# Performance work log

Measured on AMD Instinct MI355X. Metric: run time of the kernel, lower is better.

The kernel has to match this reference:

```python
import jax, jax.numpy as jnp
import numpy as np

B, N = 4, 20                        # batch, qubits
L = int(np.ceil(np.log2(N)))        # 5 layers, one 4x4 generator each


def setup_inputs():
    key = jax.random.key(0)
    k1, k2, k3, k4 = jax.random.split(key, 4)
    psi_re = jax.random.normal(k1, (B, 2 ** N), dtype=jnp.float32)
    psi_im = jax.random.normal(k2, (B, 2 ** N), dtype=jnp.float32)
    nrm = jnp.sqrt(jnp.sum(psi_re ** 2 + psi_im ** 2, axis=1, keepdims=True))
    psi_re, psi_im = psi_re / nrm, psi_im / nrm   # normalized quantum state
    H_re = jax.random.normal(k3, (L, 4, 4), dtype=jnp.float32)
    H_im = jax.random.normal(k4, (L, 4, 4), dtype=jnp.float32)
    return {"psi_re": psi_re, "psi_im": psi_im, "H_re": H_re, "H_im": H_im}


def _make_unitary(A):
    # torch.matrix_exp(A - A^H): expm of an anti-Hermitian generator via eigh
    G = A - A.conj().T
    w, V = jnp.linalg.eigh(-1j * G)            # G = i * Hermitian
    return (V * jnp.exp(1j * w)) @ V.conj().T  # expm(G), unitary


def _apply_gate(T, U4, axes):
    # contract 4x4 gate (reshaped [2,2,2,2]) onto two qubit axes of tensor T
    T = jnp.tensordot(U4, T, axes=((2, 3), axes))
    return jnp.moveaxis(T, (0, 1), axes)


def _gate_pairs(nq):
    pairs = [(2 * i, 2 * i + 1) for i in range(nq // 2)]
    if nq > 2:
        pairs += [(2 * i + 1, (2 * i + 2) % nq) for i in range(nq // 2)]
    return pairs


def _forward(psi_re, psi_im, H_re, H_im):
    psi = (psi_re + 1j * psi_im).astype(jnp.complex64).reshape((B,) + (2,) * N)
    H = (H_re + 1j * H_im).astype(jnp.complex64)
    state, is_dm, nq = psi, False, N
    for layer in range(L):
        U = _make_unitary(H[layer]).reshape(2, 2, 2, 2)
        Uc = U.conj()
        # _2local_conv: brick pattern of the same 2-qubit gate
        for (a, b) in _gate_pairs(nq):
            state = _apply_gate(state, U, (1 + a, 1 + b))
            if is_dm:  # density matrix: also apply U* on bra axes
                state = _apply_gate(state, Uc, (1 + nq + a, 1 + nq + b))
        # _2local_pool: measuring qubits 0..nq//2-1 with index shifting removes
        # the even-indexed qubits -> partial trace over them
        if nq >= 2:
            traced = [2 * i for i in range(nq // 2)]
            kept = [q for q in range(nq) if q not in traced]
            t, k = len(traced), len(kept)
            if is_dm:
                perm = (0,) + tuple(1 + q for q in kept) + tuple(1 + q for q in traced) \
                     + tuple(1 + nq + q for q in kept) + tuple(1 + nq + q for q in traced)
                r = jnp.transpose(state, perm).reshape(B, 2 ** k, 2 ** t, 2 ** k, 2 ** t)
                state = jnp.einsum('bitjt->bij', r).reshape((B,) + (2,) * k + (2,) * k)
            else:
                perm = (0,) + tuple(1 + q for q in traced) + tuple(1 + q for q in kept)
                p = jnp.transpose(state, perm).reshape(B, 2 ** t, 2 ** k)
                state = jnp.einsum('bti,btj->bij', p, p.conj()).reshape((B,) + (2,) * k + (2,) * k)
                is_dm = True
            nq = k
    # final state.measure(0): reduced 1-qubit density matrix, take P(outcome 0)
    r = state.reshape(B, 2, 2 ** (nq - 1), 2, 2 ** (nq - 1))
    rho0 = jnp.einsum('birjr->bij', r)
    return rho0[:, 0, 0].real


def reference(psi_re, psi_im, H_re, H_im):
    return _forward(psi_re, psi_im, H_re, H_im)
```

## Files before the change

kernel.cpp:

```cpp
#include <hip/hip_runtime.h>
#include <math.h>


__device__ __forceinline__ float2 cmul(float2 a, float2 b) {
  return make_float2(a.x * b.x - a.y * b.y, a.x * b.y + a.y * b.x);
}
__device__ __forceinline__ float2 cmadd(float2 acc, float2 a, float2 b) {
  acc.x = fmaf(a.x, b.x, fmaf(-a.y, b.y, acc.x));
  acc.y = fmaf(a.x, b.y, fmaf(a.y, b.x, acc.y));
  return acc;
}
__device__ __forceinline__ float2 cmaddc(float2 acc, float2 a, float2 b) {
  acc.x = fmaf(a.x, b.x, fmaf(a.y, b.y, acc.x));
  acc.y = fmaf(a.y, b.x, fmaf(-a.x, b.y, acc.y));
  return acc;
}
__device__ __forceinline__ int pad(int e) { return e + (e >> 4); }
__device__ __forceinline__ int ins(int x, int p) {
  return ((x >> p) << (p + 1)) | (x & ((1 << p) - 1));
}

__device__ __forceinline__ void gate4(float2& v0, float2& v1, float2& v2, float2& v3,
                                      const float2 (&U)[16]) {
  float2 n0 = cmul(U[0], v0);  n0 = cmadd(n0, U[1], v1);  n0 = cmadd(n0, U[2], v2);  n0 = cmadd(n0, U[3], v3);
  float2 n1 = cmul(U[4], v0);  n1 = cmadd(n1, U[5], v1);  n1 = cmadd(n1, U[6], v2);  n1 = cmadd(n1, U[7], v3);
  float2 n2 = cmul(U[8], v0);  n2 = cmadd(n2, U[9], v1);  n2 = cmadd(n2, U[10], v2); n2 = cmadd(n2, U[11], v3);
  float2 n3 = cmul(U[12], v0); n3 = cmadd(n3, U[13], v1); n3 = cmadd(n3, U[14], v2); n3 = cmadd(n3, U[15], v3);
  v0 = n0; v1 = n1; v2 = n2; v3 = n3;
}

template <int NG>
__device__ __forceinline__ void gate16n(float2 (&v)[16], const float2 (&U)[16]) {
#pragma unroll
  for (int g = 0; g < 4; g++)
    gate4(v[g * 4 + 0], v[g * 4 + 1], v[g * 4 + 2], v[g * 4 + 3], U);
#pragma unroll
  for (int lo = 0; lo < 4; lo++)
    gate4(v[lo], v[lo + 4], v[lo + 8], v[lo + 12], U);
  if (NG == 3) {
#pragma unroll
    for (int b3 = 0; b3 < 2; b3++)
#pragma unroll
      for (int b0 = 0; b0 < 2; b0++) {
        int j = b3 * 8 + b0;
        gate4(v[j], v[j + 2], v[j + 4], v[j + 6], U);
      }
  }
}

__device__ __forceinline__ void apply_gate_tile13(float2* t, const float2 (&U)[16],
                                                  int pa, int pb, int tid) {
  int p0 = pa < pb ? pa : pb;
  int p1 = pa < pb ? pb : pa;
  int m0 = (1 << p0) - 1, m1 = (1 << p1) - 1;
  int ia = 1 << pa, ib = 1 << pb;
#pragma unroll
  for (int g = tid; g < 2048; g += 512) {
    int idx = ((g & ~m0) << 1) | (g & m0);
    idx = ((idx & ~m1) << 1) | (idx & m1);
    int e0 = pad(idx), e1 = pad(idx | ib), e2 = pad(idx | ia), e3 = pad(idx | ia | ib);
    float2 v0 = t[e0], v1 = t[e1], v2 = t[e2], v3 = t[e3];
    gate4(v0, v1, v2, v3, U);
    t[e0] = v0; t[e1] = v1; t[e2] = v2; t[e3] = v3;
  }
}

template <int NG>
__device__ __forceinline__ void phase4_f(float2* t, const float2 (&U)[16],
                                         int q0, int q1, int q2, int q3,
                                         int o0, int o1, int o2, int o3, int tid) {
  int idx = ins(ins(ins(ins(tid, q0), q1), q2), q3);
  float2 v[16];
#pragma unroll
  for (int j = 0; j < 16; j++) {
    int off = ((j & 1) ? o0 : 0) + ((j & 2) ? o1 : 0) + ((j & 4) ? o2 : 0) + ((j & 8) ? o3 : 0);
    v[j] = t[pad(idx + off)];
  }
  gate16n<NG>(v, U);
#pragma unroll
  for (int j = 0; j < 16; j++) {
    int off = ((j & 1) ? o0 : 0) + ((j & 2) ? o1 : 0) + ((j & 4) ? o2 : 0) + ((j & 8) ? o3 : 0);
    t[pad(idx + off)] = v[j];
  }
}

template <int NG>
__device__ __forceinline__ void phase4_pool(float2* w, const float2 (&U)[16],
                                            int a_lo, int a_hi, int c_lo, int c_hi,
                                            int o0, int o1, int o2, int o3, int tid) {
  int uu = tid & 7, ss = (tid >> 3) & 7, t_lo = tid >> 6;
  int u = ins(ins(uu, a_lo), a_hi);
  int s = ins(ins(ss, c_lo), c_hi);
  int base = t_lo * 1120 + s * 35 + u;
  float2 v[16];
#pragma unroll
  for (int j = 0; j < 16; j++) {
    int off = ((j & 1) ? o0 : 0) + ((j & 2) ? o1 : 0) + ((j & 4) ? o2 : 0) + ((j & 8) ? o3 : 0);
    v[j] = w[base + off];
  }
  gate16n<NG>(v, U);
#pragma unroll
  for (int j = 0; j < 16; j++) {
    int off = ((j & 1) ? o0 : 0) + ((j & 2) ? o1 : 0) + ((j & 4) ? o2 : 0) + ((j & 8) ? o3 : 0);
    w[base + off] = v[j];
  }
}

__device__ __forceinline__ void pool_p3(float2* w, const float2 (&U)[16], int tid) {
#pragma unroll
  for (int it = 0; it < 2; it++) {
    int h = tid + it * 512;
    int uu = h & 7, ss = (h >> 3) & 15, t_lo = h >> 7;
    int base = t_lo * 1120 + (ss << 1) * 35 + (uu << 2);
    float2 v[8];
    v[0] = w[base];      v[1] = w[base + 1];
    v[4] = w[base + 2];  v[5] = w[base + 3];
    v[2] = w[base + 35]; v[3] = w[base + 36];
    v[6] = w[base + 37]; v[7] = w[base + 38];
    gate4(v[0], v[1], v[2], v[3], U);
    gate4(v[4], v[5], v[6], v[7], U);
    gate4(v[0], v[2], v[4], v[6], U);
    gate4(v[1], v[3], v[5], v[7], U);
    w[base] = v[0];      w[base + 1] = v[1];
    w[base + 2] = v[4];  w[base + 3] = v[5];
    w[base + 35] = v[2]; w[base + 36] = v[3];
    w[base + 37] = v[6]; w[base + 38] = v[7];
  }
}

__device__ __forceinline__ float2 expm16(const float* __restrict__ Hre,
                                         const float* __restrict__ Him,
                                         int l, int l16) {
  int r = l16 >> 2, c = l16 & 3;
  double tr = (double)Hre[l * 16 + r * 4 + c] - (double)Hre[l * 16 + c * 4 + r];
  double ti = (double)Him[l * 16 + r * 4 + c] + (double)Him[l * 16 + c * 4 + r];
  double a = sqrt(tr * tr + ti * ti);
  a += __shfl_xor(a, 1, 16);
  a += __shfl_xor(a, 2, 16);
  double nrm = fmax(a, __shfl_xor(a, 4, 16));
  nrm = fmax(nrm, __shfl_xor(nrm, 8, 16));
  int s = 0;
  while (nrm > 0.25 && s < 60) { nrm *= 0.5; s++; }
  double sc = ldexp(1.0, -s);
  tr *= sc; ti *= sc;
  double id = (r == c) ? 1.0 : 0.0;
  double er = id, ei = 0.0, pr = id, pi = 0.0;
  for (int k = 1; k <= 16; k++) {
    double qr = 0.0, qi = 0.0;
#pragma unroll
    for (int m = 0; m < 4; m++) {
      double pmr = __shfl(pr, r * 4 + m, 16);
      double pmi = __shfl(pi, r * 4 + m, 16);
      double tmr = __shfl(tr, m * 4 + c, 16);
      double tmi = __shfl(ti, m * 4 + c, 16);
      qr = fma(pmr, tmr, fma(-pmi, tmi, qr));
      qi = fma(pmr, tmi, fma(pmi, tmr, qi));
    }
    double inv = 1.0 / (double)k;
    pr = qr * inv; pi = qi * inv;
    er += pr; ei += pi;
  }
  for (int it = 0; it < s; it++) {
    double qr = 0.0, qi = 0.0;
#pragma unroll
    for (int m = 0; m < 4; m++) {
      double amr = __shfl(er, r * 4 + m, 16);
      double ami = __shfl(ei, r * 4 + m, 16);
      double bmr = __shfl(er, m * 4 + c, 16);
      double bmi = __shfl(ei, m * 4 + c, 16);
      qr = fma(amr, bmr, fma(-ami, bmi, qr));
      qi = fma(amr, bmi, fma(ami, bmr, qi));
    }
    er = qr; ei = qi;
  }
  return make_float2((float)er, (float)ei);
}

__global__ __launch_bounds__(512, 4) void l0_pass1(const float* __restrict__ pre,
                                                   const float* __restrict__ pim,
                                                   const float* __restrict__ Hre,
                                                   const float* __restrict__ Him,
                                                   float2* __restrict__ Umat,
                                                   float2* __restrict__ state) {
  extern __shared__ float2 tile[];
  __shared__ float2 Ush[16];
  int tid = threadIdx.x;
  int bid = blockIdx.x;
  int b = bid >> 7, hi = bid & 127;
  size_t base = ((size_t)b << 20) | ((size_t)hi << 13);
  for (int e4 = tid; e4 < 2048; e4 += 512) {
    int e = e4 << 2;
    float4 re = *(const float4*)&pre[base + e];
    float4 im = *(const float4*)&pim[base + e];
    int d = pad(e);
    tile[d] = make_float2(re.x, im.x);
    tile[d + 1] = make_float2(re.y, im.y);
    tile[d + 2] = make_float2(re.z, im.z);
    tile[d + 3] = make_float2(re.w, im.w);
  }
  {
    int wv = tid >> 6, g16 = (tid & 63) >> 4, l16 = tid & 15;
    int layer = (wv == 0) ? g16 : ((wv == 1 && g16 == 0) ? 4 : -1);
    if (layer == 0 || (bid == 0 && layer > 0)) {
      float2 ue = expm16(Hre, Him, layer, l16);
      if (layer == 0) Ush[l16] = ue;
      if (bid == 0) Umat[layer * 16 + l16] = ue;
    }
  }
  __syncthreads();
  float2 U[16];
#pragma unroll
  for (int k = 0; k < 16; k++) U[k] = Ush[k];
  phase4_f<3>(tile, U, 0, 1, 2, 3, 1, 2, 4, 8, tid);            __syncthreads();
  phase4_f<3>(tile, U, 4, 5, 6, 7, 16, 32, 64, 128, tid);       __syncthreads();
  phase4_f<3>(tile, U, 8, 9, 10, 11, 256, 512, 1024, 2048, tid);__syncthreads();
  phase4_f<2>(tile, U, 3, 4, 7, 8, 8, 16, 128, 256, tid);       __syncthreads();
  int hifix = ((hi & 1) << 16) | (((hi >> 1) & 1) << 6) | (((hi >> 2) & 1) << 17)
            | (((hi >> 3) & 1) << 5) | (((hi >> 4) & 1) << 18) | (((hi >> 5) & 1) << 7)
            | (((hi >> 6) & 1) << 19);
  size_t dbase = ((size_t)b << 20) | (unsigned)hifix;
  for (int e4 = tid; e4 < 2048; e4 += 512) {
    int le = e4;
    int d = ((le & 1) << 2) | (((le >> 1) & 1) << 3) | (((le >> 2) & 1) << 8)
          | (((le >> 3) & 1) << 12) | (((le >> 4) & 1) << 10) | (((le >> 5) & 1) << 13)
          | (((le >> 6) & 1) << 9) | (((le >> 7) & 1) << 14) | (((le >> 8) & 1) << 11)
          | (((le >> 9) & 1) << 15) | (((le >> 10) & 1) << 4);
    int src = pad(e4 << 2);
    float2 x0 = tile[src], x1 = tile[src + 1], x2 = tile[src + 2], x3 = tile[src + 3];
    float4* dst = (float4*)&state[dbase + d];
    dst[0] = make_float4(x0.x, x0.y, x1.x, x1.y);
    dst[1] = make_float4(x2.x, x2.y, x3.x, x3.y);
  }
}

__global__ __launch_bounds__(512, 4) void l0_pass2(const float2* __restrict__ Umat,
                                                   float2* __restrict__ state) {
  extern __shared__ float2 tile[];
  int tid = threadIdx.x;
  int bid = blockIdx.x;
  int b = bid >> 7, mid = bid & 127;
  size_t base = ((size_t)b << 20) | ((size_t)mid << 8);
  float2 U[16];
#pragma unroll
  for (int k = 0; k < 16; k++) U[k] = Umat[k];
  for (int f = tid; f < 4096; f += 512) {
    int run = f >> 7, idx = f & 127;
    size_t a = base + ((size_t)run << 15) + ((size_t)idx << 1);
    float4 v = *(const float4*)&state[a];
    int d = pad(run * 256 + idx * 2);
    tile[d] = make_float2(v.x, v.y);
    tile[d + 1] = make_float2(v.z, v.w);
  }
  __syncthreads();
  phase4_f<3>(tile, U, 4, 6, 9, 10, 16, 512, 64, 1024, tid);    __syncthreads();
  phase4_f<3>(tile, U, 5, 7, 11, 12, 32, 2048, 128, 4096, tid); __syncthreads();
  phase4_f<2>(tile, U, 4, 5, 8, 10, 256, 16, 1024, 32, tid);    __syncthreads();
  apply_gate_tile13(tile, U, 0, 12, tid);                       __syncthreads();
  for (int f = tid; f < 4096; f += 512) {
    int run = f >> 7, idx = f & 127;
    size_t a = base + ((size_t)run << 15) + ((size_t)idx << 1);
    int d = pad(run * 256 + idx * 2);
    float2 x0 = tile[d], x1 = tile[d + 1];
    *(float4*)&state[a] = make_float4(x0.x, x0.y, x1.x, x1.y);
  }
}

__global__ __launch_bounds__(512, 4) void pool_l1(const float2* __restrict__ Umat,
                                                  const float2* __restrict__ state,
                                                  float2* __restrict__ partial) {
  extern __shared__ float2 w[];
  int tid = threadIdx.x;
  int bid = blockIdx.x;
  int b = bid >> 7, thi = bid & 127;
  size_t base = ((size_t)b << 20) | ((size_t)thi << 13);
  float2 U[16];
#pragma unroll
  for (int k = 0; k < 16; k++) U[k] = Umat[16 + k];
  for (int f = tid; f < 4096; f += 512) {
    int e = f << 1;
    float4 v = *(const float4*)&state[base + e];
    int u = (((e >> 8) & 1) << 1) | (((e >> 9) & 1) << 2) | (((e >> 4) & 1) << 3) | (((e >> 5) & 1) << 4);
    int s = ((e >> 2) & 1) | (((e >> 10) & 1) << 1) | (((e >> 11) & 1) << 2)
          | (((e >> 6) & 1) << 3) | (((e >> 7) & 1) << 4);
    int t = ((e >> 1) & 1) | (((e >> 3) & 1) << 1) | (((e >> 12) & 1) << 2);
    int c = t * 1120 + s * 35 + u;
    w[c] = make_float2(v.x, v.y);
    w[c + 1] = make_float2(v.z, v.w);
  }
  __syncthreads();
  phase4_pool<3>(w, U, 3, 4, 3, 4, 8, 280, 16, 560, tid); __syncthreads();
  phase4_pool<3>(w, U, 1, 2, 1, 2, 2, 70, 4, 140, tid);   __syncthreads();
  pool_p3(w, U, tid);                                     __syncthreads();
  phase4_pool<2>(w, U, 0, 3, 2, 4, 140, 8, 560, 1, tid);  __syncthreads();
  int wv = tid >> 6, lane = tid & 63;
  int u0 = (lane >> 3) << 2, v0 = (lane & 7) << 2;
  float2 acc[4][4];
#pragma unroll
  for (int i = 0; i < 4; i++)
#pragma unroll
    for (int j = 0; j < 4; j++) acc[i][j] = make_float2(0.f, 0.f);
  {
    int tb = wv * 1120;
#pragma unroll 4
    for (int s = 0; s < 32; s++) {
      int row = tb + s * 35;
      float2 x[4], y[4];
#pragma unroll
      for (int i = 0; i < 4; i++) { x[i] = w[row + u0 + i]; y[i] = w[row + v0 + i]; }
#pragma unroll
      for (int i = 0; i < 4; i++)
#pragma unroll
        for (int j = 0; j < 4; j++) acc[i][j] = cmaddc(acc[i][j], x[i], y[j]);
    }
  }
  __syncthreads();
  if (wv > 0) {
#pragma unroll
    for (int i = 0; i < 4; i++)
#pragma unroll
      for (int j = 0; j < 4; j++)
        w[(wv - 1) * 1024 + (u0 + i) * 32 + (v0 + j)] = acc[i][j];
  }
  __syncthreads();
  if (wv == 0) {
    float2* outp = partial + ((size_t)bid << 10);
#pragma unroll
    for (int i = 0; i < 4; i++)
#pragma unroll
      for (int j = 0; j < 4; j++) {
        float2 a = acc[i][j];
#pragma unroll
        for (int k = 0; k < 7; k++) {
          float2 o = w[k * 1024 + (u0 + i) * 32 + (v0 + j)];
          a.x += o.x; a.y += o.y;
        }
        outp[(u0 + i) * 32 + (v0 + j)] = a;
      }
  }
}

__global__ __launch_bounds__(256) void reduce_partials(const float4* __restrict__ partial,
                                                       float4* __restrict__ inter) {
  int blk = blockIdx.x;
  int b = blk >> 3, q = blk & 7;
  int tid = threadIdx.x;
  for (int o = tid; o < 512; o += 256) {
    float4 acc = make_float4(0.f, 0.f, 0.f, 0.f);
#pragma unroll 4
    for (int h = 0; h < 16; h++) {
      int tile = (b * 128) + (q * 16) + h;
      float4 v = partial[(size_t)tile * 512 + o];
      acc.x += v.x; acc.y += v.y; acc.z += v.z; acc.w += v.w;
    }
    inter[(size_t)blk * 512 + o] = acc;
  }
}

__global__ __launch_bounds__(256) void finish(const float2* __restrict__ Umat,
                                              const float4* __restrict__ inter,
                                              float* __restrict__ out) {
  __shared__ float2 rho[1024];
  __shared__ float2 r3s[64];
  __shared__ float2 r4s[16];
  int tid = threadIdx.x;
  int b = blockIdx.x;
  float4* rf = (float4*)rho;
  for (int f = tid; f < 512; f += 256) {
    float4 acc = make_float4(0.f, 0.f, 0.f, 0.f);
#pragma unroll
    for (int q = 0; q < 8; q++) {
      float4 v = inter[(size_t)(b * 8 + q) * 512 + f];
      acc.x += v.x; acc.y += v.y; acc.z += v.z; acc.w += v.w;
    }
    rf[f] = acc;
  }
  __syncthreads();

  float2 U[16], Uc[16];
#pragma unroll
  for (int k = 0; k < 16; k++) { U[k] = Umat[32 + k]; Uc[k] = make_float2(U[k].x, -U[k].y); }
  const int gl2[4][2] = {{4,3},{2,1},{3,2},{1,0}};
#pragma unroll
  for (int gi = 0; gi < 4; gi++) {
    int pa = gl2[gi][0], pb = gl2[gi][1];
    int p0 = pa < pb ? pa : pb, p1 = pa < pb ? pb : pa;
    int m0 = (1 << p0) - 1, m1 = (1 << p1) - 1;
    int ia = 1 << pa, ib = 1 << pb;
    {
      int j = tid >> 3, g = tid & 7;
      int idx = ((g & ~m0) << 1) | (g & m0);
      idx = ((idx & ~m1) << 1) | (idx & m1);
      float2 v0 = rho[idx * 32 + j], v1 = rho[(idx | ib) * 32 + j];
      float2 v2 = rho[(idx | ia) * 32 + j], v3 = rho[(idx | ia | ib) * 32 + j];
      gate4(v0, v1, v2, v3, U);
      rho[idx * 32 + j] = v0; rho[(idx | ib) * 32 + j] = v1;
      rho[(idx | ia) * 32 + j] = v2; rho[(idx | ia | ib) * 32 + j] = v3;
    }
    __syncthreads();
    {
      int i = tid >> 3, g = tid & 7;
      int idx = ((g & ~m0) << 1) | (g & m0);
      idx = ((idx & ~m1) << 1) | (idx & m1);
      float2 v0 = rho[i * 32 + idx], v1 = rho[i * 32 + (idx | ib)];
      float2 v2 = rho[i * 32 + (idx | ia)], v3 = rho[i * 32 + (idx | ia | ib)];
      gate4(v0, v1, v2, v3, Uc);
      rho[i * 32 + idx] = v0; rho[i * 32 + (idx | ib)] = v1;
      rho[i * 32 + (idx | ia)] = v2; rho[i * 32 + (idx | ia | ib)] = v3;
    }
    __syncthreads();
  }
  if (tid < 64) {
    int u = tid >> 3, v = tid & 7;
    float2 acc = {0.f, 0.f};
#pragma unroll
    for (int s = 0; s < 4; s++) {
      int iu = ((s >> 1) << 4) | ((u >> 2) << 3) | ((s & 1) << 2) | (((u >> 1) & 1) << 1) | (u & 1);
      int iv = ((s >> 1) << 4) | ((v >> 2) << 3) | ((s & 1) << 2) | (((v >> 1) & 1) << 1) | (v & 1);
      float2 x = rho[iu * 32 + iv];
      acc.x += x.x; acc.y += x.y;
    }
    r3s[u * 8 + v] = acc;
  }
  __syncthreads();

#pragma unroll
  for (int k = 0; k < 16; k++) { U[k] = Umat[48 + k]; Uc[k] = make_float2(U[k].x, -U[k].y); }
  const int gl3[2][2] = {{2,1},{1,0}};
#pragma unroll
  for (int gi = 0; gi < 2; gi++) {
    int pa = gl3[gi][0], pb = gl3[gi][1];
    int p0 = pa < pb ? pa : pb, p1 = pa < pb ? pb : pa;
    int m0 = (1 << p0) - 1, m1 = (1 << p1) - 1;
    int ia = 1 << pa, ib = 1 << pb;
    if (tid < 16) {
      int j = tid >> 1, g = tid & 1;
      int idx = ((g & ~m0) << 1) | (g & m0);
      idx = ((idx & ~m1) << 1) | (idx & m1);
      float2 v0 = r3s[idx * 8 + j], v1 = r3s[(idx | ib) * 8 + j];
      float2 v2 = r3s[(idx | ia) * 8 + j], v3 = r3s[(idx | ia | ib) * 8 + j];
      gate4(v0, v1, v2, v3, U);
      r3s[idx * 8 + j] = v0; r3s[(idx | ib) * 8 + j] = v1;
      r3s[(idx | ia) * 8 + j] = v2; r3s[(idx | ia | ib) * 8 + j] = v3;
    }
    __syncthreads();
    if (tid < 16) {
      int i = tid >> 1, g = tid & 1;
      int idx = ((g & ~m0) << 1) | (g & m0);
      idx = ((idx & ~m1) << 1) | (idx & m1);
      float2 v0 = r3s[i * 8 + idx], v1 = r3s[i * 8 + (idx | ib)];
      float2 v2 = r3s[i * 8 + (idx | ia)], v3 = r3s[i * 8 + (idx | ia | ib)];
      gate4(v0, v1, v2, v3, Uc);
      r3s[i * 8 + idx] = v0; r3s[i * 8 + (idx | ib)] = v1;
      r3s[i * 8 + (idx | ia)] = v2; r3s[i * 8 + (idx | ia | ib)] = v3;
    }
    __syncthreads();
  }
  if (tid < 16) {
    int u = tid >> 2, v = tid & 3;
    float2 acc = {0.f, 0.f};
#pragma unroll
    for (int s = 0; s < 2; s++) {
      float2 x = r3s[((s << 2) | u) * 8 + ((s << 2) | v)];
      acc.x += x.x; acc.y += x.y;
    }
    r4s[u * 4 + v] = acc;
  }
  __syncthreads();

#pragma unroll
  for (int k = 0; k < 16; k++) { U[k] = Umat[64 + k]; Uc[k] = make_float2(U[k].x, -U[k].y); }
  if (tid < 4) {
    int j = tid;
    float2 v0 = r4s[0 * 4 + j], v1 = r4s[1 * 4 + j], v2 = r4s[2 * 4 + j], v3 = r4s[3 * 4 + j];
    gate4(v0, v1, v2, v3, U);
    r4s[0 * 4 + j] = v0; r4s[1 * 4 + j] = v1; r4s[2 * 4 + j] = v2; r4s[3 * 4 + j] = v3;
  }
  __syncthreads();
  if (tid < 4) {
    int i = tid;
    float2 v0 = r4s[i * 4 + 0], v1 = r4s[i * 4 + 1], v2 = r4s[i * 4 + 2], v3 = r4s[i * 4 + 3];
    gate4(v0, v1, v2, v3, Uc);
    r4s[i * 4 + 0] = v0; r4s[i * 4 + 1] = v1; r4s[i * 4 + 2] = v2; r4s[i * 4 + 3] = v3;
  }
  __syncthreads();
  if (tid == 0) out[b] = r4s[0].x + r4s[10].x;
}

extern "C" void kernel_launch(void* const* d_in, const int* in_sizes, int n_in,
                              void* d_out, int out_size, void* d_ws, size_t ws_size,
                              hipStream_t stream) {
  const float* psi_re = (const float*)d_in[0];
  const float* psi_im = (const float*)d_in[1];
  const float* H_re = (const float*)d_in[2];
  const float* H_im = (const float*)d_in[3];
  float* out = (float*)d_out;

  char* ws = (char*)d_ws;
  float2* Umat = (float2*)ws;
  float2* state = (float2*)(ws + 4096);
  float* partial = (float*)(ws + 4096 + ((size_t)1 << 25));
  float* inter = (float*)(ws + 4096 + ((size_t)1 << 25) + ((size_t)1 << 22));

  const size_t LDS_L0 = 8704 * sizeof(float2);
  const size_t LDS_POOL = 8960 * sizeof(float2);

  hipLaunchKernelGGL(l0_pass1, dim3(512), dim3(512), LDS_L0, stream,
                     psi_re, psi_im, H_re, H_im, Umat, state);
  hipLaunchKernelGGL(l0_pass2, dim3(512), dim3(512), LDS_L0, stream,
                     (const float2*)Umat, state);
  hipLaunchKernelGGL(pool_l1, dim3(512), dim3(512), LDS_POOL, stream,
                     (const float2*)Umat, (const float2*)state, (float2*)partial);
  hipLaunchKernelGGL(reduce_partials, dim3(32), dim3(256), 0, stream,
                     (const float4*)partial, (float4*)inter);
  hipLaunchKernelGGL(finish, dim3(4), dim3(256), 0, stream,
                     (const float2*)Umat, (const float4*)inter, out);
}
```

Before: 172.4 us.

## Use packed float2 vector FMA complex math and atomic partial reduction

Complex arithmetic moves to a clang ext_vector float2 type built on elementwise FMA, so the compiler can emit packed FP32 (v_pk_fma_f32) instructions in the gate kernels. The separate reduce_partials kernel is removed. pool_l1 now atomically adds each block's partial density matrix into 32 accumulation slots, which l0_pass1 zeroes at start, and finish sums 8 slots per batch. This drops a kernel launch and the partial-buffer round trip, at the cost of float atomic contention and a nondeterministic summation order.

```diff
diff --git a/kernel.cpp b/kernel.cpp
--- a/kernel.cpp
+++ b/kernel.cpp
@@ -2,35 +2,39 @@
 #include <math.h>
 
 
-__device__ __forceinline__ float2 cmul(float2 a, float2 b) {
-  return make_float2(a.x * b.x - a.y * b.y, a.x * b.y + a.y * b.x);
-}
-__device__ __forceinline__ float2 cmadd(float2 acc, float2 a, float2 b) {
-  acc.x = fmaf(a.x, b.x, fmaf(-a.y, b.y, acc.x));
-  acc.y = fmaf(a.x, b.y, fmaf(a.y, b.x, acc.y));
-  return acc;
-}
-__device__ __forceinline__ float2 cmaddc(float2 acc, float2 a, float2 b) {
-  acc.x = fmaf(a.x, b.x, fmaf(a.y, b.y, acc.x));
-  acc.y = fmaf(a.y, b.x, fmaf(-a.x, b.y, acc.y));
-  return acc;
-}
+typedef float cpx __attribute__((ext_vector_type(2)));
+
+__device__ __forceinline__ cpx mkc(float x, float y) { cpx r; r.x = x; r.y = y; return r; }
+
+__device__ __forceinline__ cpx cmul(cpx a, cpx b) {
+  cpx r = a.xx * b;
+  return __builtin_elementwise_fma(mkc(-a.y, a.y), b.yx, r);
+}
+__device__ __forceinline__ cpx cmadd(cpx acc, cpx a, cpx b) {
+  acc = __builtin_elementwise_fma(a.xx, b, acc);
+  return __builtin_elementwise_fma(mkc(-a.y, a.y), b.yx, acc);
+}
+__device__ __forceinline__ cpx cmaddc(cpx acc, cpx a, cpx b) {
+  acc = __builtin_elementwise_fma(a.xx, mkc(b.x, -b.y), acc);
+  return __builtin_elementwise_fma(a.yy, b.yx, acc);
+}
+
 __device__ __forceinline__ int pad(int e) { return e + (e >> 4); }
 __device__ __forceinline__ int ins(int x, int p) {
   return ((x >> p) << (p + 1)) | (x & ((1 << p) - 1));
 }
 
-__device__ __forceinline__ void gate4(float2& v0, float2& v1, float2& v2, float2& v3,
-                                      const float2 (&U)[16]) {
-  float2 n0 = cmul(U[0], v0);  n0 = cmadd(n0, U[1], v1);  n0 = cmadd(n0, U[2], v2);  n0 = cmadd(n0, U[3], v3);
-  float2 n1 = cmul(U[4], v0);  n1 = cmadd(n1, U[5], v1);  n1 = cmadd(n1, U[6], v2);  n1 = cmadd(n1, U[7], v3);
-  float2 n2 = cmul(U[8], v0);  n2 = cmadd(n2, U[9], v1);  n2 = cmadd(n2, U[10], v2); n2 = cmadd(n2, U[11], v3);
-  float2 n3 = cmul(U[12], v0); n3 = cmadd(n3, U[13], v1); n3 = cmadd(n3, U[14], v2); n3 = cmadd(n3, U[15], v3);
+__device__ __forceinline__ void gate4(cpx& v0, cpx& v1, cpx& v2, cpx& v3,
+                                      const cpx (&U)[16]) {
+  cpx n0 = cmul(U[0], v0);  n0 = cmadd(n0, U[1], v1);  n0 = cmadd(n0, U[2], v2);  n0 = cmadd(n0, U[3], v3);
+  cpx n1 = cmul(U[4], v0);  n1 = cmadd(n1, U[5], v1);  n1 = cmadd(n1, U[6], v2);  n1 = cmadd(n1, U[7], v3);
+  cpx n2 = cmul(U[8], v0);  n2 = cmadd(n2, U[9], v1);  n2 = cmadd(n2, U[10], v2); n2 = cmadd(n2, U[11], v3);
+  cpx n3 = cmul(U[12], v0); n3 = cmadd(n3, U[13], v1); n3 = cmadd(n3, U[14], v2); n3 = cmadd(n3, U[15], v3);
   v0 = n0; v1 = n1; v2 = n2; v3 = n3;
 }
 
 template <int NG>
-__device__ __forceinline__ void gate16n(float2 (&v)[16], const float2 (&U)[16]) {
+__device__ __forceinline__ void gate16n(cpx (&v)[16], const cpx (&U)[16]) {
 #pragma unroll
   for (int g = 0; g < 4; g++)
     gate4(v[g * 4 + 0], v[g * 4 + 1], v[g * 4 + 2], v[g * 4 + 3], U);
@@ -48,7 +52,7 @@
   }
 }
 
-__device__ __forceinline__ void apply_gate_tile13(float2* t, const float2 (&U)[16],
+__device__ __forceinline__ void apply_gate_tile13(cpx* t, const cpx (&U)[16],
                                                   int pa, int pb, int tid) {
   int p0 = pa < pb ? pa : pb;
   int p1 = pa < pb ? pb : pa;
@@ -59,18 +63,18 @@
     int idx = ((g & ~m0) << 1) | (g & m0);
     idx = ((idx & ~m1) << 1) | (idx & m1);
     int e0 = pad(idx), e1 = pad(idx | ib), e2 = pad(idx | ia), e3 = pad(idx | ia | ib);
-    float2 v0 = t[e0], v1 = t[e1], v2 = t[e2], v3 = t[e3];
+    cpx v0 = t[e0], v1 = t[e1], v2 = t[e2], v3 = t[e3];
     gate4(v0, v1, v2, v3, U);
     t[e0] = v0; t[e1] = v1; t[e2] = v2; t[e3] = v3;
   }
 }
 
 template <int NG>
-__device__ __forceinline__ void phase4_f(float2* t, const float2 (&U)[16],
+__device__ __forceinline__ void phase4_f(cpx* t, const cpx (&U)[16],
                                          int q0, int q1, int q2, int q3,
                                          int o0, int o1, int o2, int o3, int tid) {
   int idx = ins(ins(ins(ins(tid, q0), q1), q2), q3);
-  float2 v[16];
+  cpx v[16];
 #pragma unroll
   for (int j = 0; j < 16; j++) {
     int off = ((j & 1) ? o0 : 0) + ((j & 2) ? o1 : 0) + ((j & 4) ? o2 : 0) + ((j & 8) ? o3 : 0);
@@ -85,14 +89,14 @@
 }
 
 template <int NG>
-__device__ __forceinline__ void phase4_pool(float2* w, const float2 (&U)[16],
+__device__ __forceinline__ void phase4_pool(cpx* w, const cpx (&U)[16],
                                             int a_lo, int a_hi, int c_lo, int c_hi,
                                             int o0, int o1, int o2, int o3, int tid) {
   int uu = tid & 7, ss = (tid >> 3) & 7, t_lo = tid >> 6;
   int u = ins(ins(uu, a_lo), a_hi);
   int s = ins(ins(ss, c_lo), c_hi);
   int base = t_lo * 1120 + s * 35 + u;
-  float2 v[16];
+  cpx v[16];
 #pragma unroll
   for (int j = 0; j < 16; j++) {
     int off = ((j & 1) ? o0 : 0) + ((j & 2) ? o1 : 0) + ((j & 4) ? o2 : 0) + ((j & 8) ? o3 : 0);
@@ -106,13 +110,13 @@
   }
 }
 
-__device__ __forceinline__ void pool_p3(float2* w, const float2 (&U)[16], int tid) {
+__device__ __forceinline__ void pool_p3(cpx* w, const cpx (&U)[16], int tid) {
 #pragma unroll
   for (int it = 0; it < 2; it++) {
     int h = tid + it * 512;
     int uu = h & 7, ss = (h >> 3) & 15, t_lo = h >> 7;
     int base = t_lo * 1120 + (ss << 1) * 35 + (uu << 2);
-    float2 v[8];
+    cpx v[8];
     v[0] = w[base];      v[1] = w[base + 1];
     v[4] = w[base + 2];  v[5] = w[base + 3];
     v[2] = w[base + 35]; v[3] = w[base + 36];
@@ -128,9 +132,9 @@
   }
 }
 
-__device__ __forceinline__ float2 expm16(const float* __restrict__ Hre,
-                                         const float* __restrict__ Him,
-                                         int l, int l16) {
+__device__ __forceinline__ cpx expm16(const float* __restrict__ Hre,
+                                      const float* __restrict__ Him,
+                                      int l, int l16) {
   int r = l16 >> 2, c = l16 & 3;
   double tr = (double)Hre[l * 16 + r * 4 + c] - (double)Hre[l * 16 + c * 4 + r];
   double ti = (double)Him[l * 16 + r * 4 + c] + (double)Him[l * 16 + c * 4 + r];
@@ -173,42 +177,44 @@
     }
     er = qr; ei = qi;
   }
-  return make_float2((float)er, (float)ei);
+  return mkc((float)er, (float)ei);
 }
 
 __global__ __launch_bounds__(512, 4) void l0_pass1(const float* __restrict__ pre,
                                                    const float* __restrict__ pim,
                                                    const float* __restrict__ Hre,
                                                    const float* __restrict__ Him,
-                                                   float2* __restrict__ Umat,
-                                                   float2* __restrict__ state) {
-  extern __shared__ float2 tile[];
-  __shared__ float2 Ush[16];
+                                                   cpx* __restrict__ Umat,
+                                                   cpx* __restrict__ state,
+                                                   float4* __restrict__ accz) {
+  extern __shared__ cpx tile[];
+  __shared__ cpx Ush[16];
   int tid = threadIdx.x;
   int bid = blockIdx.x;
   int b = bid >> 7, hi = bid & 127;
   size_t base = ((size_t)b << 20) | ((size_t)hi << 13);
+  if (tid < 32) accz[(bid << 5) | tid] = make_float4(0.f, 0.f, 0.f, 0.f);
   for (int e4 = tid; e4 < 2048; e4 += 512) {
     int e = e4 << 2;
     float4 re = *(const float4*)&pre[base + e];
     float4 im = *(const float4*)&pim[base + e];
     int d = pad(e);
-    tile[d] = make_float2(re.x, im.x);
-    tile[d + 1] = make_float2(re.y, im.y);
-    tile[d + 2] = make_float2(re.z, im.z);
-    tile[d + 3] = make_float2(re.w, im.w);
+    tile[d] = mkc(re.x, im.x);
+    tile[d + 1] = mkc(re.y, im.y);
+    tile[d + 2] = mkc(re.z, im.z);
+    tile[d + 3] = mkc(re.w, im.w);
   }
   {
     int wv = tid >> 6, g16 = (tid & 63) >> 4, l16 = tid & 15;
     int layer = (wv == 0) ? g16 : ((wv == 1 && g16 == 0) ? 4 : -1);
     if (layer == 0 || (bid == 0 && layer > 0)) {
-      float2 ue = expm16(Hre, Him, layer, l16);
+      cpx ue = expm16(Hre, Him, layer, l16);
       if (layer == 0) Ush[l16] = ue;
       if (bid == 0) Umat[layer * 16 + l16] = ue;
     }
   }
   __syncthreads();
-  float2 U[16];
+  cpx U[16];
 #pragma unroll
   for (int k = 0; k < 16; k++) U[k] = Ush[k];
   phase4_f<3>(tile, U, 0, 1, 2, 3, 1, 2, 4, 8, tid);            __syncthreads();
@@ -226,21 +232,21 @@
           | (((le >> 6) & 1) << 9) | (((le >> 7) & 1) << 14) | (((le >> 8) & 1) << 11)
           | (((le >> 9) & 1) << 15) | (((le >> 10) & 1) << 4);
     int src = pad(e4 << 2);
-    float2 x0 = tile[src], x1 = tile[src + 1], x2 = tile[src + 2], x3 = tile[src + 3];
+    cpx x0 = tile[src], x1 = tile[src + 1], x2 = tile[src + 2], x3 = tile[src + 3];
     float4* dst = (float4*)&state[dbase + d];
     dst[0] = make_float4(x0.x, x0.y, x1.x, x1.y);
     dst[1] = make_float4(x2.x, x2.y, x3.x, x3.y);
   }
 }
 
-__global__ __launch_bounds__(512, 4) void l0_pass2(const float2* __restrict__ Umat,
-                                                   float2* __restrict__ state) {
-  extern __shared__ float2 tile[];
+__global__ __launch_bounds__(512, 4) void l0_pass2(const cpx* __restrict__ Umat,
+                                                   cpx* __restrict__ state) {
+  extern __shared__ cpx tile[];
   int tid = threadIdx.x;
   int bid = blockIdx.x;
   int b = bid >> 7, mid = bid & 127;
   size_t base = ((size_t)b << 20) | ((size_t)mid << 8);
-  float2 U[16];
+  cpx U[16];
 #pragma unroll
   for (int k = 0; k < 16; k++) U[k] = Umat[k];
   for (int f = tid; f < 4096; f += 512) {
@@ -248,8 +254,8 @@
     size_t a = base + ((size_t)run << 15) + ((size_t)idx << 1);
     float4 v = *(const float4*)&state[a];
     int d = pad(run * 256 + idx * 2);
-    tile[d] = make_float2(v.x, v.y);
-    tile[d + 1] = make_float2(v.z, v.w);
+    tile[d] = mkc(v.x, v.y);
+    tile[d + 1] = mkc(v.z, v.w);
   }
   __syncthreads();
   phase4_f<3>(tile, U, 4, 6, 9, 10, 16, 512, 64, 1024, tid);    __syncthreads();
@@ -260,20 +266,20 @@
     int run = f >> 7, idx = f & 127;
     size_t a = base + ((size_t)run << 15) + ((size_t)idx << 1);
     int d = pad(run * 256 + idx * 2);
-    float2 x0 = tile[d], x1 = tile[d + 1];
+    cpx x0 = tile[d], x1 = tile[d + 1];
     *(float4*)&state[a] = make_float4(x0.x, x0.y, x1.x, x1.y);
   }
 }
 
-__global__ __launch_bounds__(512, 4) void pool_l1(const float2* __restrict__ Umat,
-                                                  const float2* __restrict__ state,
-                                                  float2* __restrict__ partial) {
-  extern __shared__ float2 w[];
+__global__ __launch_bounds__(512, 4) void pool_l1(const cpx* __restrict__ Umat,
+                                                  const cpx* __restrict__ state,
+                                                  float* __restrict__ accbuf) {
+  extern __shared__ cpx w[];
   int tid = threadIdx.x;
   int bid = blockIdx.x;
   int b = bid >> 7, thi = bid & 127;
   size_t base = ((size_t)b << 20) | ((size_t)thi << 13);
-  float2 U[16];
+  cpx U[16];
 #pragma unroll
   for (int k = 0; k < 16; k++) U[k] = Umat[16 + k];
   for (int f = tid; f < 4096; f += 512) {
@@ -284,8 +290,8 @@
           | (((e >> 6) & 1) << 3) | (((e >> 7) & 1) << 4);
     int t = ((e >> 1) & 1) | (((e >> 3) & 1) << 1) | (((e >> 12) & 1) << 2);
     int c = t * 1120 + s * 35 + u;
-    w[c] = make_float2(v.x, v.y);
-    w[c + 1] = make_float2(v.z, v.w);
+    w[c] = mkc(v.x, v.y);
+    w[c + 1] = mkc(v.z, v.w);
   }
   __syncthreads();
   phase4_pool<3>(w, U, 3, 4, 3, 4, 8, 280, 16, 560, tid); __syncthreads();
@@ -294,17 +300,17 @@
   phase4_pool<2>(w, U, 0, 3, 2, 4, 140, 8, 560, 1, tid);  __syncthreads();
   int wv = tid >> 6, lane = tid & 63;
   int u0 = (lane >> 3) << 2, v0 = (lane & 7) << 2;
-  float2 acc[4][4];
+  cpx acc[4][4];
 #pragma unroll
   for (int i = 0; i < 4; i++)
 #pragma unroll
-    for (int j = 0; j < 4; j++) acc[i][j] = make_float2(0.f, 0.f);
+    for (int j = 0; j < 4; j++) acc[i][j] = mkc(0.f, 0.f);
   {
     int tb = wv * 1120;
 #pragma unroll 4
     for (int s = 0; s < 32; s++) {
       int row = tb + s * 35;
-      float2 x[4], y[4];
+      cpx x[4], y[4];
 #pragma unroll
       for (int i = 0; i < 4; i++) { x[i] = w[row + u0 + i]; y[i] = w[row + v0 + i]; }
 #pragma unroll
@@ -323,62 +329,47 @@
   }
   __syncthreads();
   if (wv == 0) {
-    float2* outp = partial + ((size_t)bid << 10);
+    float* dst = accbuf + ((size_t)((b << 3) | (thi & 7)) << 11);
 #pragma unroll
     for (int i = 0; i < 4; i++)
 #pragma unroll
       for (int j = 0; j < 4; j++) {
-        float2 a = acc[i][j];
+        cpx a = acc[i][j];
 #pragma unroll
         for (int k = 0; k < 7; k++) {
-          float2 o = w[k * 1024 + (u0 + i) * 32 + (v0 + j)];
+          cpx o = w[k * 1024 + (u0 + i) * 32 + (v0 + j)];
           a.x += o.x; a.y += o.y;
         }
-        outp[(u0 + i) * 32 + (v0 + j)] = a;
+        int off = (((u0 + i) << 5) | (v0 + j)) << 1;
+        atomicAdd(dst + off, a.x);
+        atomicAdd(dst + off + 1, a.y);
       }
   }
 }
 
-__global__ __launch_bounds__(256) void reduce_partials(const float4* __restrict__ partial,
-                                                       float4* __restrict__ inter) {
-  int blk = blockIdx.x;
-  int b = blk >> 3, q = blk & 7;
-  int tid = threadIdx.x;
-  for (int o = tid; o < 512; o += 256) {
-    float4 acc = make_float4(0.f, 0.f, 0.f, 0.f);
-#pragma unroll 4
-    for (int h = 0; h < 16; h++) {
-      int tile = (b * 128) + (q * 16) + h;
-      float4 v = partial[(size_t)tile * 512 + o];
-      acc.x += v.x; acc.y += v.y; acc.z += v.z; acc.w += v.w;
-    }
-    inter[(size_t)blk * 512 + o] = acc;
-  }
-}
-
-__global__ __launch_bounds__(256) void finish(const float2* __restrict__ Umat,
-                                              const float4* __restrict__ inter,
+__global__ __launch_bounds__(256) void finish(const cpx* __restrict__ Umat,
+                                              const float4* __restrict__ accv,
                                               float* __restrict__ out) {
-  __shared__ float2 rho[1024];
-  __shared__ float2 r3s[64];
-  __shared__ float2 r4s[16];
+  __shared__ cpx rho[1024];
+  __shared__ cpx r3s[64];
+  __shared__ cpx r4s[16];
   int tid = threadIdx.x;
   int b = blockIdx.x;
   float4* rf = (float4*)rho;
   for (int f = tid; f < 512; f += 256) {
     float4 acc = make_float4(0.f, 0.f, 0.f, 0.f);
 #pragma unroll
-    for (int q = 0; q < 8; q++) {
-      float4 v = inter[(size_t)(b * 8 + q) * 512 + f];
+    for (int r = 0; r < 8; r++) {
+      float4 v = accv[(size_t)((b << 3) | r) * 512 + f];
       acc.x += v.x; acc.y += v.y; acc.z += v.z; acc.w += v.w;
     }
     rf[f] = acc;
   }
   __syncthreads();
 
-  float2 U[16], Uc[16];
-#pragma unroll
-  for (int k = 0; k < 16; k++) { U[k] = Umat[32 + k]; Uc[k] = make_float2(U[k].x, -U[k].y); }
+  cpx U[16], Uc[16];
+#pragma unroll
+  for (int k = 0; k < 16; k++) { U[k] = Umat[32 + k]; Uc[k] = mkc(U[k].x, -U[k].y); }
   const int gl2[4][2] = {{4,3},{2,1},{3,2},{1,0}};
 #pragma unroll
   for (int gi = 0; gi < 4; gi++) {
@@ -390,8 +381,8 @@
       int j = tid >> 3, g = tid & 7;
       int idx = ((g & ~m0) << 1) | (g & m0);
       idx = ((idx & ~m1) << 1) | (idx & m1);
-      float2 v0 = rho[idx * 32 + j], v1 = rho[(idx | ib) * 32 + j];
-      float2 v2 = rho[(idx | ia) * 32 + j], v3 = rho[(idx | ia | ib) * 32 + j];
+      cpx v0 = rho[idx * 32 + j], v1 = rho[(idx | ib) * 32 + j];
+      cpx v2 = rho[(idx | ia) * 32 + j], v3 = rho[(idx | ia | ib) * 32 + j];
       gate4(v0, v1, v2, v3, U);
       rho[idx * 32 + j] = v0; rho[(idx | ib) * 32 + j] = v1;
       rho[(idx | ia) * 32 + j] = v2; rho[(idx | ia | ib) * 32 + j] = v3;
@@ -401,8 +392,8 @@
       int i = tid >> 3, g = tid & 7;
       int idx = ((g & ~m0) << 1) | (g & m0);
       idx = ((idx & ~m1) << 1) | (idx & m1);
-      float2 v0 = rho[i * 32 + idx], v1 = rho[i * 32 + (idx | ib)];
-      float2 v2 = rho[i * 32 + (idx | ia)], v3 = rho[i * 32 + (idx | ia | ib)];
+      cpx v0 = rho[i * 32 + idx], v1 = rho[i * 32 + (idx | ib)];
+      cpx v2 = rho[i * 32 + (idx | ia)], v3 = rho[i * 32 + (idx | ia | ib)];
       gate4(v0, v1, v2, v3, Uc);
       rho[i * 32 + idx] = v0; rho[i * 32 + (idx | ib)] = v1;
       rho[i * 32 + (idx | ia)] = v2; rho[i * 32 + (idx | ia | ib)] = v3;
@@ -411,12 +402,12 @@
   }
   if (tid < 64) {
     int u = tid >> 3, v = tid & 7;
-    float2 acc = {0.f, 0.f};
+    cpx acc = mkc(0.f, 0.f);
 #pragma unroll
     for (int s = 0; s < 4; s++) {
       int iu = ((s >> 1) << 4) | ((u >> 2) << 3) | ((s & 1) << 2) | (((u >> 1) & 1) << 1) | (u & 1);
       int iv = ((s >> 1) << 4) | ((v >> 2) << 3) | ((s & 1) << 2) | (((v >> 1) & 1) << 1) | (v & 1);
-      float2 x = rho[iu * 32 + iv];
+      cpx x = rho[iu * 32 + iv];
       acc.x += x.x; acc.y += x.y;
     }
     r3s[u * 8 + v] = acc;
@@ -424,7 +415,7 @@
   __syncthreads();
 
 #pragma unroll
-  for (int k = 0; k < 16; k++) { U[k] = Umat[48 + k]; Uc[k] = make_float2(U[k].x, -U[k].y); }
+  for (int k = 0; k < 16; k++) { U[k] = Umat[48 + k]; Uc[k] = mkc(U[k].x, -U[k].y); }
   const int gl3[2][2] = {{2,1},{1,0}};
 #pragma unroll
   for (int gi = 0; gi < 2; gi++) {
@@ -436,8 +427,8 @@
       int j = tid >> 1, g = tid & 1;
       int idx = ((g & ~m0) << 1) | (g & m0);
       idx = ((idx & ~m1) << 1) | (idx & m1);
-      float2 v0 = r3s[idx * 8 + j], v1 = r3s[(idx | ib) * 8 + j];
-      float2 v2 = r3s[(idx | ia) * 8 + j], v3 = r3s[(idx | ia | ib) * 8 + j];
+      cpx v0 = r3s[idx * 8 + j], v1 = r3s[(idx | ib) * 8 + j];
+      cpx v2 = r3s[(idx | ia) * 8 + j], v3 = r3s[(idx | ia | ib) * 8 + j];
       gate4(v0, v1, v2, v3, U);
       r3s[idx * 8 + j] = v0; r3s[(idx | ib) * 8 + j] = v1;
       r3s[(idx | ia) * 8 + j] = v2; r3s[(idx | ia | ib) * 8 + j] = v3;
@@ -447,8 +438,8 @@
       int i = tid >> 1, g = tid & 1;
       int idx = ((g & ~m0) << 1) | (g & m0);
       idx = ((idx & ~m1) << 1) | (idx & m1);
-      float2 v0 = r3s[i * 8 + idx], v1 = r3s[i * 8 + (idx | ib)];
-      float2 v2 = r3s[i * 8 + (idx | ia)], v3 = r3s[i * 8 + (idx | ia | ib)];
+      cpx v0 = r3s[i * 8 + idx], v1 = r3s[i * 8 + (idx | ib)];
+      cpx v2 = r3s[i * 8 + (idx | ia)], v3 = r3s[i * 8 + (idx | ia | ib)];
       gate4(v0, v1, v2, v3, Uc);
       r3s[i * 8 + idx] = v0; r3s[i * 8 + (idx | ib)] = v1;
       r3s[i * 8 + (idx | ia)] = v2; r3s[i * 8 + (idx | ia | ib)] = v3;
@@ -457,10 +448,10 @@
   }
   if (tid < 16) {
     int u = tid >> 2, v = tid & 3;
-    float2 acc = {0.f, 0.f};
+    cpx acc = mkc(0.f, 0.f);
 #pragma unroll
     for (int s = 0; s < 2; s++) {
-      float2 x = r3s[((s << 2) | u) * 8 + ((s << 2) | v)];
+      cpx x = r3s[((s << 2) | u) * 8 + ((s << 2) | v)];
       acc.x += x.x; acc.y += x.y;
     }
     r4s[u * 4 + v] = acc;
@@ -468,17 +459,17 @@
   __syncthreads();
 
 #pragma unroll
-  for (int k = 0; k < 16; k++) { U[k] = Umat[64 + k]; Uc[k] = make_float2(U[k].x, -U[k].y); }
+  for (int k = 0; k < 16; k++) { U[k] = Umat[64 + k]; Uc[k] = mkc(U[k].x, -U[k].y); }
   if (tid < 4) {
     int j = tid;
-    float2 v0 = r4s[0 * 4 + j], v1 = r4s[1 * 4 + j], v2 = r4s[2 * 4 + j], v3 = r4s[3 * 4 + j];
+    cpx v0 = r4s[0 * 4 + j], v1 = r4s[1 * 4 + j], v2 = r4s[2 * 4 + j], v3 = r4s[3 * 4 + j];
     gate4(v0, v1, v2, v3, U);
     r4s[0 * 4 + j] = v0; r4s[1 * 4 + j] = v1; r4s[2 * 4 + j] = v2; r4s[3 * 4 + j] = v3;
   }
   __syncthreads();
   if (tid < 4) {
     int i = tid;
-    float2 v0 = r4s[i * 4 + 0], v1 = r4s[i * 4 + 1], v2 = r4s[i * 4 + 2], v3 = r4s[i * 4 + 3];
+    cpx v0 = r4s[i * 4 + 0], v1 = r4s[i * 4 + 1], v2 = r4s[i * 4 + 2], v3 = r4s[i * 4 + 3];
     gate4(v0, v1, v2, v3, Uc);
     r4s[i * 4 + 0] = v0; r4s[i * 4 + 1] = v1; r4s[i * 4 + 2] = v2; r4s[i * 4 + 3] = v3;
   }
@@ -496,22 +487,19 @@
   float* out = (float*)d_out;
 
   char* ws = (char*)d_ws;
-  float2* Umat = (float2*)ws;
-  float2* state = (float2*)(ws + 4096);
-  float* partial = (float*)(ws + 4096 + ((size_t)1 << 25));
-  float* inter = (float*)(ws + 4096 + ((size_t)1 << 25) + ((size_t)1 << 22));
-
-  const size_t LDS_L0 = 8704 * sizeof(float2);
-  const size_t LDS_POOL = 8960 * sizeof(float2);
+  cpx* Umat = (cpx*)ws;
+  float* accb = (float*)(ws + 4096);
+  cpx* state = (cpx*)(ws + ((size_t)1 << 19));
+
+  const size_t LDS_L0 = 8704 * sizeof(cpx);
+  const size_t LDS_POOL = 8960 * sizeof(cpx);
 
   hipLaunchKernelGGL(l0_pass1, dim3(512), dim3(512), LDS_L0, stream,
-                     psi_re, psi_im, H_re, H_im, Umat, state);
+                     psi_re, psi_im, H_re, H_im, Umat, state, (float4*)accb);
   hipLaunchKernelGGL(l0_pass2, dim3(512), dim3(512), LDS_L0, stream,
-                     (const float2*)Umat, state);
+                     (const cpx*)Umat, state);
   hipLaunchKernelGGL(pool_l1, dim3(512), dim3(512), LDS_POOL, stream,
-                     (const float2*)Umat, (const float2*)state, (float2*)partial);
-  hipLaunchKernelGGL(reduce_partials, dim3(32), dim3(256), 0, stream,
-                     (const float4*)partial, (float4*)inter);
+                     (const cpx*)Umat, (const cpx*)state, accb);
   hipLaunchKernelGGL(finish, dim3(4), dim3(256), 0, stream,
-                     (const float2*)Umat, (const float4*)inter, out);
-}
+                     (const cpx*)Umat, (const float4*)accb, out);
+}
```

Measured after the change: 180.7 us. 1.05x slower.
